# Optimization experiments

Hardware: AMD Instinct MI355X
Metric: run time of the kernel (lower is better)

Reference implementation:

```python
import jax, jax.numpy as jnp
from jax import lax
import numpy as np

PH, PW = 5, 5      # patch_shape; forced to 5x5 by the (batch, F, 27) reshape in AdaptiveConv
F = 32             # adaptive conv output channels
SCALE = 4          # super-resolution upscale factor


def conv2d(x, w, b, padding):
    # x: NCHW, w: OIHW
    y = lax.conv_general_dilated(x, w, (1, 1), padding,
                                 dimension_numbers=('NCHW', 'OIHW', 'NCHW'))
    return y + b[None, :, None, None]


def space_to_batch(x):
    # non-overlapping PHxPW tiles, order (batch, tile_row, tile_col) like the torch loops
    B, C, H, W = x.shape
    hn, wn = H // PH, W // PW
    p = x.reshape(B, C, hn, PH, wn, PW).transpose(0, 2, 4, 1, 3, 5)
    return p.reshape(B * hn * wn, C, PH, PW), (B, hn, wn)


def batch_to_space(p, meta):
    B, hn, wn = meta
    C = p.shape[1]
    out = p.reshape(B, hn, wn, C, PH, PW).transpose(0, 3, 1, 4, 2, 5)
    return out.reshape(B, C, hn * PH, wn * PW)


def unfold3(x):
    # torch F.unfold(x, 3, padding=1): (N, C*9, L) channel-major (c, kh, kw); return (N, L, C*9)
    N, C, H, W = x.shape
    xp = jnp.pad(x, ((0, 0), (0, 0), (1, 1), (1, 1)))
    cols = jnp.stack([xp[:, :, i:i + H, j:j + W]
                      for i in range(3) for j in range(3)], axis=2)  # (N, C, 9, H, W)
    return cols.reshape(N, C * 9, H * W).transpose(0, 2, 1)


def pixel_shuffle(x, r):
    B, Cr2, H, W = x.shape
    C = Cr2 // (r * r)
    return (x.reshape(B, C, r, r, H, W)
             .transpose(0, 1, 4, 2, 5, 3)
             .reshape(B, C, H * r, W * r))


def setup_inputs() -> dict:
    key = jax.random.key(0)
    ks = jax.random.split(key, 13)
    rn = lambda k, shape, s=0.05: jax.random.normal(k, shape, jnp.float32) * s
    return dict(
        x=jax.random.normal(ks[0], (2, 3, 360, 640), jnp.float32),
        w_feat=rn(ks[1], (256, 3, 3, 3)),        b_feat=rn(ks[2], (256,)),
        w_kern=rn(ks[3], (27 * F, 256, 3, 3)),   b_kern=rn(ks[4], (27 * F,)),
        w_badp=rn(ks[5], (F, 256, 3, 3)),        b_badp=rn(ks[6], (F,)),
        w1=rn(ks[7], (128, F, 5, 5)),            b1=rn(ks[8], (128,)),
        w2=rn(ks[9], (32, 128, 3, 3)),           b2=rn(ks[10], (32,)),
        w3=rn(ks[11], (3 * SCALE * SCALE, 32, 3, 3)), b3=rn(ks[12], (3 * SCALE * SCALE,)),
    )


def reference(x, w_feat, b_feat, w_kern, b_kern, w_badp, b_badp,
              w1, b1, w2, b2, w3, b3):
    patches, meta = space_to_batch(x)                        # (N, 3, 5, 5)
    N = patches.shape[0]
    # AdaptiveConv: per-patch dynamic 3x3 conv
    feat = jax.nn.relu(conv2d(patches, w_feat, b_feat, 'VALID'))   # (N, 256, 3, 3)
    kern = conv2d(feat, w_kern, b_kern, 'VALID')                   # (N, 27F, 1, 1)
    kern = kern.reshape(N, F, 27).transpose(0, 2, 1)               # (N, 27, F)
    xu = unfold3(patches)                                          # (N, 25, 27)
    out = jnp.einsum('nlk,nkf->nlf', xu, kern)                     # (N, 25, F)
    out = out.transpose(0, 2, 1).reshape(N, F, PH, PW)
    bias = conv2d(feat, w_badp, b_badp, 'VALID')                   # (N, F, 1, 1)
    out = jax.nn.relu(out + bias)
    sp = batch_to_space(out, meta)                                 # (B, F, H, W)
    # RegularConv stack
    h = jax.nn.relu(conv2d(sp, w1, b1, 'SAME'))
    h = jax.nn.relu(conv2d(h, w2, b2, 'SAME'))
    h = conv2d(h, w3, b3, 'SAME')                                  # (B, 3*r*r, H, W)
    return pixel_shuffle(h, SCALE)                                 # (B, 3, H*r, W*r)
```

## Files before the change

### kernel.cpp

```cpp
#include <hip/hip_runtime.h>
#include <stdint.h>

typedef unsigned short ushort;
typedef __bf16 bf16x8 __attribute__((ext_vector_type(8)));
typedef float f32x4 __attribute__((ext_vector_type(4)));
typedef ushort ushort8 __attribute__((ext_vector_type(8)));
typedef ushort us4 __attribute__((ext_vector_type(4)));

__device__ __forceinline__ float bf2f(ushort u) {
  union { unsigned int i; float f; } v; v.i = ((unsigned int)u) << 16; return v.f;
}
__device__ __forceinline__ ushort f2bf(float f) {
  union { float f; unsigned int i; } v; v.f = f;
  unsigned int r = v.i + 0x7fffu + ((v.i >> 16) & 1u);
  return (ushort)(r >> 16);
}
__device__ __forceinline__ void glds16(const ushort* g, ushort* l) {
  __builtin_amdgcn_global_load_lds(
      (const __attribute__((address_space(1))) void*)g,
      (__attribute__((address_space(3))) void*)l, 16, 0, 0);
}

#define VMB(N)                                                  \
  do {                                                          \
    asm volatile("s_waitcnt vmcnt(" #N ")" ::: "memory");       \
    __builtin_amdgcn_s_barrier();                               \
    __builtin_amdgcn_sched_barrier(0);                          \
  } while (0)

__global__ __launch_bounds__(256) void pack_kernel(
    const float* __restrict__ w_kern, const float* __restrict__ b_kern,
    const float* __restrict__ w_badp, const float* __restrict__ b_badp,
    ushort* __restrict__ Bt, float* __restrict__ bias896) {
  int idx = blockIdx.x * 256 + threadIdx.x;
  const int total = 896 * 2304;
  if (idx < total) {
    int o = idx / 2304, k = idx - o * 2304;
    int c = k & 255, pos = k >> 8;
    float v = (o < 864) ? w_kern[(o * 256 + c) * 9 + pos]
                        : w_badp[((o - 864) * 256 + c) * 9 + pos];
    Bt[idx] = f2bf(v);
  } else if (idx < total + 896) {
    int o = idx - total;
    bias896[o] = (o < 864) ? b_kern[o] : b_badp[o - 864];
  }
}

__global__ __launch_bounds__(256) void pack2_kernel(
    const float* __restrict__ w1, const float* __restrict__ w2,
    const float* __restrict__ w3, ushort* __restrict__ wp1,
    ushort* __restrict__ wp2, ushort* __restrict__ wp3) {
  int idx = blockIdx.x * 256 + threadIdx.x;
  if (idx < 102400) {
    int t = idx >> 12, rm = idx & 4095, o = rm >> 5, c = rm & 31;
    wp1[idx] = f2bf(w1[(o * 32 + c) * 25 + t]);
  } else if (idx < 102400 + 36864) {
    int j = idx - 102400;
    int t = j >> 12, rm = j & 4095, o = rm >> 7, c = rm & 127;
    wp2[j] = f2bf(w2[(o * 128 + c) * 9 + t]);
  } else if (idx < 102400 + 36864 + 13824) {
    int j = idx - 139264;
    int t = j / 1536, rm = j - t * 1536, o = rm >> 5, c = rm & 31;
    wp3[j] = f2bf(w3[(o * 32 + c) * 9 + t]);
  }
}

__global__ __launch_bounds__(256) void feat_kernel(
    const float* __restrict__ x, const float* __restrict__ w_feat,
    const float* __restrict__ b_feat, ushort* __restrict__ feat) {
  __shared__ float xp[4][3][5][5];
  const int t = threadIdx.x;
  const int n0 = blockIdx.x * 4;
  for (int e = t; e < 300; e += 256) {
    int p = e / 75, rem = e - p * 75;
    int ci = rem / 25, r = rem - ci * 25, i = r / 5, j = r - i * 5;
    int n = n0 + p;
    int b = n / 9216, ph = (n >> 7) % 72, pw = n & 127;
    xp[p][ci][i][j] = x[((b * 3 + ci) * 360 + ph * 5 + i) * 640 + pw * 5 + j];
  }
  float wf[27];
#pragma unroll
  for (int m = 0; m < 27; ++m) wf[m] = w_feat[t * 27 + m];
  const float bv = b_feat[t];
  __syncthreads();
  for (int p = 0; p < 4; ++p) {
    ushort* dst = feat + (size_t)(n0 + p) * 2304 + t;
#pragma unroll
    for (int pi = 0; pi < 3; ++pi)
#pragma unroll
      for (int pj = 0; pj < 3; ++pj) {
        float acc = bv;
#pragma unroll
        for (int ci = 0; ci < 3; ++ci)
#pragma unroll
          for (int ki = 0; ki < 3; ++ki)
#pragma unroll
            for (int kj = 0; kj < 3; ++kj)
              acc = fmaf(xp[p][ci][pi + ki][pj + kj], wf[ci * 9 + ki * 3 + kj], acc);
        dst[(pi * 3 + pj) * 256] = f2bf(fmaxf(acc, 0.f));
      }
  }
}

__global__ __launch_bounds__(256) void gemm_kernel(
    const ushort* __restrict__ A, const ushort* __restrict__ Bt,
    const float* __restrict__ bias, ushort* __restrict__ C) {
  const int K = 2304, N = 896;
  __shared__ __align__(16) ushort lA[3][4096];
  __shared__ __align__(16) ushort lB[3][4096];
  const int bid = blockIdx.x;
  const int xcd = bid & 7, j = bid >> 3;
  const int mblk = xcd * 18 + j / 7, nblk = j % 7;
  const int m0 = mblk * 128, n0 = nblk * 128;
  const int t = threadIdx.x;
  const int lane = t & 63, wave = t >> 6;
  const int wm = wave >> 1, wn = wave & 1;
  const int lp = lane & 15, lk = lane >> 4;
  f32x4 acc[4][4] = {};
  const int srow = t >> 2;
  const int sslot = (t & 3) ^ ((srow >> 1) & 3);
  const ushort* gA = A + (size_t)(m0 + srow) * K + sslot * 8;
  const ushort* gB = Bt + (size_t)(n0 + srow) * K + sslot * 8;
  const int swz = lk ^ ((lp >> 1) & 3);
  const int aoff = (wm * 64 + lp) * 32 + swz * 8;
  const int boff = (wn * 64 + lp) * 32 + swz * 8;

#define KT(x) ((x) < 2304 ? (x) : 2272)
#define GSTAGE(buf, kt)                                       \
  do {                                                        \
    glds16(gA + (kt), &lA[buf][wave * 512]);                  \
    glds16(gA + 64 * K + (kt), &lA[buf][2048 + wave * 512]);  \
    glds16(gB + (kt), &lB[buf][wave * 512]);                  \
    glds16(gB + 64 * K + (kt), &lB[buf][2048 + wave * 512]);  \
  } while (0)

#define GCOMP(buf)                                                            \
  do {                                                                        \
    bf16x8 af[4], bfr[4];                                                     \
    _Pragma("unroll") for (int mi = 0; mi < 4; ++mi)                          \
        af[mi] = __builtin_bit_cast(bf16x8,                                   \
            *(const ushort8*)(&lA[buf][aoff + mi * 512]));                    \
    _Pragma("unroll") for (int ni = 0; ni < 4; ++ni)                          \
        bfr[ni] = __builtin_bit_cast(bf16x8,                                  \
            *(const ushort8*)(&lB[buf][boff + ni * 512]));                    \
    _Pragma("unroll") for (int mi = 0; mi < 4; ++mi)                          \
        _Pragma("unroll") for (int ni = 0; ni < 4; ++ni)                      \
            acc[mi][ni] = __builtin_amdgcn_mfma_f32_16x16x32_bf16(            \
                af[mi], bfr[ni], acc[mi][ni], 0, 0, 0);                       \
  } while (0)

  GSTAGE(0, 0);
  GSTAGE(1, 32);
#pragma unroll 1
  for (int i = 0; i < 72; i += 3) {
    VMB(4); GSTAGE(2, KT((i + 2) * 32)); GCOMP(0);
    VMB(4); GSTAGE(0, KT((i + 3) * 32)); GCOMP(1);
    VMB(4); GSTAGE(1, KT((i + 4) * 32)); GCOMP(2);
  }
#undef GSTAGE
#undef GCOMP
#undef KT

#pragma unroll
  for (int ni = 0; ni < 4; ++ni) {
    int col = n0 + wn * 64 + ni * 16 + lp;
    float bv = bias[col];
#pragma unroll
    for (int mi = 0; mi < 4; ++mi) {
      int row0 = m0 + wm * 64 + mi * 16 + lk * 4;
#pragma unroll
      for (int r = 0; r < 4; ++r)
        C[(size_t)(row0 + r) * N + col] = f2bf(acc[mi][ni][r] + bv);
    }
  }
}

__global__ __launch_bounds__(256) void apply_kernel(
    const float* __restrict__ x, const ushort* __restrict__ kernbias,
    ushort* __restrict__ sp) {
  __shared__ float xp[8][3][7][7];
  __shared__ ushort outl[8][32][25];
  const int t = threadIdx.x;
  const int n0 = blockIdx.x * 8;
  const int b = n0 / 9216, ph = (n0 >> 7) % 72, pw0 = n0 & 127;
  for (int e = t; e < 8 * 3 * 49; e += 256) ((float*)xp)[e] = 0.f;
  __syncthreads();
  for (int e = t; e < 600; e += 256) {
    int p = e / 75, rem = e - p * 75;
    int ci = rem / 25, r = rem - ci * 25, i = r / 5, j = r - i * 5;
    xp[p][ci][i + 1][j + 1] = x[((b * 3 + ci) * 360 + ph * 5 + i) * 640 + (pw0 + p) * 5 + j];
  }
  __syncthreads();
  const int p = t >> 5, f = t & 31;
  const int n = n0 + p;
  float kk[27];
#pragma unroll
  for (int k = 0; k < 27; ++k) kk[k] = bf2f(kernbias[(size_t)n * 896 + f * 27 + k]);
  const float bv = bf2f(kernbias[(size_t)n * 896 + 864 + f]);
  for (int l = 0; l < 25; ++l) {
    int li = l / 5, lj = l - li * 5;
    float s = bv;
#pragma unroll
    for (int k = 0; k < 27; ++k) {
      int ci = k / 9, rm = k - ci * 9, ki = rm / 3, kj = rm - ki * 3;
      s = fmaf(xp[p][ci][li + ki][lj + kj], kk[k], s);
    }
    outl[p][f][l] = f2bf(fmaxf(s, 0.f));
  }
  __syncthreads();
  for (int e = t; e < 6400; e += 256) {
    int f2 = e & 31;
    int idx = e >> 5;
    int i = idx / 40, c40 = idx - i * 40;
    int pp = c40 / 5, j = c40 - pp * 5;
    sp[(((size_t)b * 360 + ph * 5 + i) * 640 + pw0 * 5 + c40) * 32 + f2] = outl[pp][f2][i * 5 + j];
  }
}

__global__ __launch_bounds__(512, 4) void conv1_kernel(
    const ushort* __restrict__ sp, const ushort* __restrict__ wp1,
    const float* __restrict__ b1, ushort* __restrict__ h1) {
  __shared__ ushort8 lin[8 * 4 * 69];
  __shared__ ushort8 wbuf[4][512];
  const int t = threadIdx.x;
  const int lane = t & 63, wave = t >> 6;
  const int wh = wave >> 1, wn = wave & 1;
  const int lp = lane & 15, lk = lane >> 4;
  const int w0 = blockIdx.x * 64, h0 = blockIdx.y * 4, b = blockIdx.z;
  const int srcoff = (t >> 2) * 32 + (((t & 3) ^ ((t >> 3) & 3)) * 8);
#define WSTAGE(bf, tap) glds16(wp1 + (tap) * 4096 + srcoff, (ushort*)&wbuf[bf][wave * 64])
  WSTAGE(0, 0);
  WSTAGE(1, 1);
  WSTAGE(2, 2);
  for (int u = t; u < 8 * 4 * 68; u += 512) {
    int c8 = u & 3, rest = u >> 2;
    int wx = rest % 68, r = rest / 68;
    int gh = h0 - 2 + r, gw = w0 - 2 + wx;
    ushort8 v = {};
    if ((unsigned)gh < 360u && (unsigned)gw < 640u)
      v = *(const ushort8*)(sp + (((size_t)b * 360 + gh) * 640 + gw) * 32 + c8 * 8);
    lin[(r * 4 + c8) * 69 + wx] = v;
  }
  __syncthreads();

  f32x4 acc[4][4] = {};
  const int wswz = lk ^ ((lp >> 1) & 3);
#pragma unroll
  for (int tp = 0; tp < 25; ++tp) {
    VMB(2);
    {
      const int tn = (tp + 3 < 25) ? tp + 3 : 24;
      WSTAGE((tp + 3) & 3, tn);
    }
    const int ki = tp / 5, kj = tp % 5;
    const ushort8* wb8 = wbuf[tp & 3];
    bf16x8 W[4], Af[4];
#pragma unroll
    for (int nf = 0; nf < 4; ++nf)
      W[nf] = __builtin_bit_cast(bf16x8, wb8[(wn * 64 + nf * 16 + lp) * 4 + wswz]);
    const int ab = (wh + ki) * 276 + lk * 69 + lp + kj;
#pragma unroll
    for (int mf = 0; mf < 4; ++mf)
      Af[mf] = __builtin_bit_cast(bf16x8, lin[ab + mf * 16]);
#pragma unroll
    for (int mf = 0; mf < 4; ++mf)
#pragma unroll
      for (int nf = 0; nf < 4; ++nf)
        acc[mf][nf] = __builtin_amdgcn_mfma_f32_16x16x32_bf16(W[nf], Af[mf], acc[mf][nf], 0, 0, 0);
  }
#undef WSTAGE

  const int h = h0 + wh;
#pragma unroll
  for (int nf = 0; nf < 4; ++nf) {
    const int oc0 = wn * 64 + nf * 16 + lk * 4;
    f32x4 bv = *(const f32x4*)(b1 + oc0);
#pragma unroll
    for (int mf = 0; mf < 4; ++mf) {
      const int w = w0 + mf * 16 + lp;
      us4 pk;
#pragma unroll
      for (int r = 0; r < 4; ++r) pk[r] = f2bf(fmaxf(acc[mf][nf][r] + bv[r], 0.f));
      *(us4*)(&h1[(((size_t)b * 360 + h) * 640 + w) * 128 + oc0]) = pk;
    }
  }
}

__device__ __forceinline__ void c2_load(ushort8* stg, const ushort* __restrict__ h1,
                                        int t, int b, int h0, int w0, int cb) {
#pragma unroll
  for (int j = 0; j < 7; ++j) {
    int u = t + j * 256;
    ushort8 v = {};
    if (u < 1584) {
      int r = u / 264, rem = u - r * 264;
      int c8 = rem / 66, wx = rem - c8 * 66;
      int gh = h0 - 1 + r, gw = w0 - 1 + wx;
      if ((unsigned)gh < 360u && (unsigned)gw < 640u)
        v = *(const ushort8*)(h1 + (((size_t)b * 360 + gh) * 640 + gw) * 128 + cb * 32 + c8 * 8);
    }
    stg[j] = v;
  }
}
__device__ __forceinline__ void c2_write(const ushort8* stg, ushort8* buf, int t) {
#pragma unroll
  for (int j = 0; j < 7; ++j) {
    int u = t + j * 256;
    if (u < 1584) {
      int r = u / 264, rem = u - r * 264;
      int c8 = rem / 66, wx = rem - c8 * 66;
      buf[c8 * 414 + r * 69 + wx] = stg[j];
    }
  }
}
__device__ __forceinline__ void c2_compute(const ushort8* buf, const ushort* __restrict__ wp2,
                                           int cb, int wave, int lp, int lk, f32x4 acc[4][2]) {
#pragma unroll
  for (int ki = 0; ki < 3; ++ki) {
    const int rb = lk * 414 + (wave + ki) * 69;
#pragma unroll
    for (int kj = 0; kj < 3; ++kj) {
      const int tap = ki * 3 + kj;
      bf16x8 bfr[2];
#pragma unroll
      for (int nf = 0; nf < 2; ++nf) {
        ushort8 tmp = *(const ushort8*)(wp2 + tap * 4096 + nf * 2048 + lp * 128 + cb * 32 + lk * 8);
        bfr[nf] = __builtin_bit_cast(bf16x8, tmp);
      }
      bf16x8 afr[4];
#pragma unroll
      for (int mf = 0; mf < 4; ++mf)
        afr[mf] = __builtin_bit_cast(bf16x8, buf[rb + lp + mf * 16 + kj]);
#pragma unroll
      for (int mf = 0; mf < 4; ++mf)
#pragma unroll
        for (int nf = 0; nf < 2; ++nf)
          acc[mf][nf] = __builtin_amdgcn_mfma_f32_16x16x32_bf16(bfr[nf], afr[mf], acc[mf][nf], 0, 0, 0);
    }
  }
}

__global__ __launch_bounds__(256) void conv2_kernel(
    const ushort* __restrict__ h1, const ushort* __restrict__ wp2,
    const float* __restrict__ b2, ushort* __restrict__ h2) {
  __shared__ ushort8 lin[2][4 * 414];
  const int t = threadIdx.x;
  const int lane = t & 63, wave = t >> 6;
  const int lp = lane & 15, lk = lane >> 4;
  const int w0 = blockIdx.x * 64, h0 = blockIdx.y * 4, b = blockIdx.z;
  f32x4 acc[4][2] = {};
  ushort8 stg[7];
  c2_load(stg, h1, t, b, h0, w0, 0);
#pragma unroll
  for (int it = 0; it < 5; ++it) {
    __syncthreads();
    if (it < 4) c2_write(stg, lin[it & 1], t);
    if (it < 3) c2_load(stg, h1, t, b, h0, w0, it + 1);
    if (it >= 1) c2_compute(lin[(it - 1) & 1], wp2, it - 1, wave, lp, lk, acc);
  }
  const int h = h0 + wave;
#pragma unroll
  for (int nf = 0; nf < 2; ++nf) {
    const int oc0 = nf * 16 + lk * 4;
    f32x4 bv = *(const f32x4*)(b2 + oc0);
#pragma unroll
    for (int mf = 0; mf < 4; ++mf) {
      const int w = w0 + mf * 16 + lp;
      us4 pk;
#pragma unroll
      for (int r = 0; r < 4; ++r) pk[r] = f2bf(fmaxf(acc[mf][nf][r] + bv[r], 0.f));
      *(us4*)(&h2[(((size_t)b * 360 + h) * 640 + w) * 32 + oc0]) = pk;
    }
  }
}

__global__ __launch_bounds__(256) void conv3_kernel(
    const ushort* __restrict__ h2, const ushort* __restrict__ wp3,
    const float* __restrict__ b3, float* __restrict__ out) {
  __shared__ ushort8 lin[4 * 4 * 67];
  const int t = threadIdx.x;
  const int lane = t & 63, wave = t >> 6;
  const int wh = wave & 1, wm = wave >> 1;
  const int lp = lane & 15, lk = lane >> 4;
  const int w0 = blockIdx.x * 64, h0 = blockIdx.y * 2, b = blockIdx.z;
  for (int u = t; u < 4 * 4 * 66; u += 256) {
    int c8 = u & 3, rest = u >> 2;
    int wx = rest % 66, r = rest / 66;
    int gh = h0 - 1 + r, gw = w0 - 1 + wx;
    ushort8 v = {};
    if (gh >= 0 && gh < 360 && gw >= 0 && gw < 640)
      v = *(const ushort8*)(h2 + (((size_t)b * 360 + gh) * 640 + gw) * 32 + c8 * 8);
    lin[(r * 4 + c8) * 67 + wx] = v;
  }
  __syncthreads();
  f32x4 acc[2][3] = {};
  const int abase = lk * 67 + wm * 32 + lp;
  const ushort* wbase = wp3 + lp * 32 + lk * 8;
#pragma unroll
  for (int ki = 0; ki < 3; ++ki) {
#pragma unroll
    for (int kj = 0; kj < 3; ++kj) {
      const int tap = ki * 3 + kj;
      bf16x8 bfr[3];
#pragma unroll
      for (int nf = 0; nf < 3; ++nf) {
        ushort8 tmp = *(const ushort8*)(wbase + (size_t)tap * 1536 + nf * 512);
        bfr[nf] = __builtin_bit_cast(bf16x8, tmp);
      }
      bf16x8 afr[2];
#pragma unroll
      for (int mf = 0; mf < 2; ++mf)
        afr[mf] = __builtin_bit_cast(bf16x8, lin[(wh + ki) * 268 + abase + mf * 16 + kj]);
#pragma unroll
      for (int mf = 0; mf < 2; ++mf)
#pragma unroll
        for (int nf = 0; nf < 3; ++nf)
          acc[mf][nf] = __builtin_amdgcn_mfma_f32_16x16x32_bf16(bfr[nf], afr[mf], acc[mf][nf], 0, 0, 0);
    }
  }
  const int h = h0 + wh;
#pragma unroll
  for (int nf = 0; nf < 3; ++nf) {
    f32x4 bv = *(const f32x4*)(b3 + nf * 16 + lk * 4);
#pragma unroll
    for (int mf = 0; mf < 2; ++mf) {
      const int w = w0 + wm * 32 + mf * 16 + lp;
      f32x4 o;
#pragma unroll
      for (int r = 0; r < 4; ++r) o[r] = acc[mf][nf][r] + bv[r];
      *(f32x4*)(&out[(((size_t)b * 3 + nf) * 1440 + h * 4 + lk) * 2560 + (size_t)w * 4]) = o;
    }
  }
}

extern "C" void kernel_launch(void* const* d_in, const int* in_sizes, int n_in,
                              void* d_out, int out_size, void* d_ws, size_t ws_size,
                              hipStream_t stream) {
  const float* x      = (const float*)d_in[0];
  const float* w_feat = (const float*)d_in[1];
  const float* b_feat = (const float*)d_in[2];
  const float* w_kern = (const float*)d_in[3];
  const float* b_kern = (const float*)d_in[4];
  const float* w_badp = (const float*)d_in[5];
  const float* b_badp = (const float*)d_in[6];
  const float* w1 = (const float*)d_in[7];
  const float* b1 = (const float*)d_in[8];
  const float* w2 = (const float*)d_in[9];
  const float* b2 = (const float*)d_in[10];
  const float* w3 = (const float*)d_in[11];
  const float* b3 = (const float*)d_in[12];

  char* ws = (char*)d_ws;
  ushort* feat     = (ushort*)(ws);
  ushort* h1       = (ushort*)(ws);
  ushort* kernbias = (ushort*)(ws + 117964800);
  ushort* h2       = (ushort*)(ws + 117964800);
  ushort* wp1      = (ushort*)(ws + 147456000);
  ushort* wp2      = (ushort*)(ws + 147660800);
  ushort* wp3      = (ushort*)(ws + 147734528);
  ushort* sp       = (ushort*)(ws + 150994944);
  ushort* Bt       = (ushort*)(ws + 180486144);
  float*  bias896  = (float*)(ws + 184614912);

  pack_kernel<<<(896 * 2304 + 896 + 255) / 256, 256, 0, stream>>>(
      w_kern, b_kern, w_badp, b_badp, Bt, bias896);
  feat_kernel<<<4608, 256, 0, stream>>>(x, w_feat, b_feat, feat);
  gemm_kernel<<<1008, 256, 0, stream>>>(feat, Bt, bias896, kernbias);
  apply_kernel<<<2304, 256, 0, stream>>>(x, kernbias, sp);
  pack2_kernel<<<598, 256, 0, stream>>>(w1, w2, w3, wp1, wp2, wp3);
  conv1_kernel<<<dim3(10, 90, 2), 512, 0, stream>>>(sp, wp1, b1, h1);
  conv2_kernel<<<dim3(10, 90, 2), 256, 0, stream>>>(h1, wp2, b2, h2);
  conv3_kernel<<<dim3(10, 180, 2), 256, 0, stream>>>(h2, wp3, b3, (float*)d_out);
}
```

Baseline: 448.2 us.

## Stage per-patch kernels through LDS and deepen conv2 load pipeline

In apply_kernel, each block now copies its 8 patches' kernel/bias rows into shared memory with coalesced loads, so threads no longer gather strided global reads directly. In conv2_kernel, the four input chunks are loaded with two register staging buffers, keeping two global loads in flight ahead of the MFMA compute on double-buffered LDS. The cost is more shared memory per block in apply_kernel and more registers in conv2, which may lower occupancy.

```diff
diff --git a/kernel.cpp b/kernel.cpp
--- a/kernel.cpp
+++ b/kernel.cpp
@@ -180,10 +180,12 @@
     ushort* __restrict__ sp) {
   __shared__ float xp[8][3][7][7];
   __shared__ ushort outl[8][32][25];
+  __shared__ ushort klds[8 * 896];
   const int t = threadIdx.x;
   const int n0 = blockIdx.x * 8;
   const int b = n0 / 9216, ph = (n0 >> 7) % 72, pw0 = n0 & 127;
   for (int e = t; e < 8 * 3 * 49; e += 256) ((float*)xp)[e] = 0.f;
+  for (int e = t; e < 7168; e += 256) klds[e] = kernbias[(size_t)n0 * 896 + e];
   __syncthreads();
   for (int e = t; e < 600; e += 256) {
     int p = e / 75, rem = e - p * 75;
@@ -192,11 +194,10 @@
   }
   __syncthreads();
   const int p = t >> 5, f = t & 31;
-  const int n = n0 + p;
   float kk[27];
 #pragma unroll
-  for (int k = 0; k < 27; ++k) kk[k] = bf2f(kernbias[(size_t)n * 896 + f * 27 + k]);
-  const float bv = bf2f(kernbias[(size_t)n * 896 + 864 + f]);
+  for (int k = 0; k < 27; ++k) kk[k] = bf2f(klds[p * 896 + f * 27 + k]);
+  const float bv = bf2f(klds[p * 896 + 864 + f]);
   for (int l = 0; l < 25; ++l) {
     int li = l / 5, lj = l - li * 5;
     float s = bv;
@@ -349,15 +350,24 @@
   const int lp = lane & 15, lk = lane >> 4;
   const int w0 = blockIdx.x * 64, h0 = blockIdx.y * 4, b = blockIdx.z;
   f32x4 acc[4][2] = {};
-  ushort8 stg[7];
-  c2_load(stg, h1, t, b, h0, w0, 0);
-#pragma unroll
-  for (int it = 0; it < 5; ++it) {
-    __syncthreads();
-    if (it < 4) c2_write(stg, lin[it & 1], t);
-    if (it < 3) c2_load(stg, h1, t, b, h0, w0, it + 1);
-    if (it >= 1) c2_compute(lin[(it - 1) & 1], wp2, it - 1, wave, lp, lk, acc);
-  }
+  ushort8 stgA[7], stgB[7];
+  c2_load(stgA, h1, t, b, h0, w0, 0);
+  c2_load(stgB, h1, t, b, h0, w0, 1);
+  c2_write(stgA, lin[0], t);
+  c2_load(stgA, h1, t, b, h0, w0, 2);
+  __syncthreads();
+  c2_write(stgB, lin[1], t);
+  c2_load(stgB, h1, t, b, h0, w0, 3);
+  c2_compute(lin[0], wp2, 0, wave, lp, lk, acc);
+  __syncthreads();
+  c2_write(stgA, lin[0], t);
+  c2_compute(lin[1], wp2, 1, wave, lp, lk, acc);
+  __syncthreads();
+  c2_write(stgB, lin[1], t);
+  c2_compute(lin[0], wp2, 2, wave, lp, lk, acc);
+  __syncthreads();
+  c2_compute(lin[1], wp2, 3, wave, lp, lk, acc);
+
   const int h = h0 + wave;
 #pragma unroll
   for (int nf = 0; nf < 2; ++nf) {
```

After: 453.5 us. About the same (+1.2%).
